# Kernel tuning notes

Hardware: AMD Instinct MI355X
Metric: run time of the kernel (lower is better)

Reference implementation:

```python
import jax, jax.numpy as jnp
import numpy as np

N_EMBD = 1024
N_HEADS = 16
B, T = 4, 2048
EPS = 1e-5


def setup_inputs() -> dict:
    key = jax.random.key(0)
    ks = jax.random.split(key, 8)
    C = N_EMBD
    s = 0.02
    return {
        "x": jax.random.normal(ks[0], (B, T, C), dtype=jnp.float32),
        "ln1_w": jnp.ones((C,), jnp.float32),
        "ln1_b": jnp.zeros((C,), jnp.float32),
        "qkv_w": jax.random.normal(ks[1], (C, 3 * C), jnp.float32) * s,
        "qkv_b": jnp.zeros((3 * C,), jnp.float32),
        "proj_w": jax.random.normal(ks[2], (C, C), jnp.float32) * s,
        "proj_b": jnp.zeros((C,), jnp.float32),
        "ln2_w": jnp.ones((C,), jnp.float32),
        "ln2_b": jnp.zeros((C,), jnp.float32),
        "ff_w1": jax.random.normal(ks[3], (C, 4 * C), jnp.float32) * s,
        "ff_b1": jnp.zeros((4 * C,), jnp.float32),
        "ff_w2": jax.random.normal(ks[4], (4 * C, C), jnp.float32) * s,
        "ff_b2": jnp.zeros((C,), jnp.float32),
    }


def _layernorm(x, w, b):
    mu = jnp.mean(x, axis=-1, keepdims=True)
    var = jnp.mean(jnp.square(x - mu), axis=-1, keepdims=True)
    return (x - mu) * jax.lax.rsqrt(var + EPS) * w + b


def _block(x, ln1_w, ln1_b, qkv_w, qkv_b, proj_w, proj_b,
           ln2_w, ln2_b, ff_w1, ff_b1, ff_w2, ff_b2):
    Bb, Tt, C = x.shape
    hd = C // N_HEADS
    h = _layernorm(x, ln1_w, ln1_b)
    qkv = h @ qkv_w + qkv_b  # [B,T,3C]
    q, k, v = jnp.split(qkv, 3, axis=-1)
    q = q.reshape(Bb, Tt, N_HEADS, hd)
    k = k.reshape(Bb, Tt, N_HEADS, hd)
    v = v.reshape(Bb, Tt, N_HEADS, hd)
    # NOTE: original scales by 1/sqrt(C) (full embed dim), not 1/sqrt(head_dim)
    att = jnp.einsum("bqhd,bkhd->bhqk", q, k) * (1.0 / C ** 0.5)
    causal = jnp.tril(jnp.ones((Tt, Tt), dtype=bool))
    att = jnp.where(causal[None, None], att, -jnp.inf)
    att = jax.nn.softmax(att, axis=-1)
    y = jnp.einsum("bhqk,bkhd->bqhd", att, v).reshape(Bb, Tt, C)
    x = x + y @ proj_w + proj_b
    h2 = _layernorm(x, ln2_w, ln2_b)
    ff = jax.nn.relu(h2 @ ff_w1 + ff_b1) @ ff_w2 + ff_b2
    return x + ff


def reference(x, ln1_w, ln1_b, qkv_w, qkv_b, proj_w, proj_b,
              ln2_w, ln2_b, ff_w1, ff_b1, ff_w2, ff_b2):
    return _block(x, ln1_w, ln1_b, qkv_w, qkv_b, proj_w, proj_b,
                  ln2_w, ln2_b, ff_w1, ff_b1, ff_w2, ff_b2)
```

## Files before the change

kernel.cpp:

```cpp
#include <hip/hip_runtime.h>


typedef __attribute__((ext_vector_type(8))) short shortx8;
typedef __attribute__((ext_vector_type(4))) float floatx4;

__device__ __forceinline__ short f2bf(float f) {
  unsigned u = __builtin_bit_cast(unsigned, f);
  u = (u + 0x7fffu + ((u >> 16) & 1u)) >> 16;
  return (short)u;
}
__device__ __forceinline__ float bf2f(short s) {
  return __builtin_bit_cast(float, (unsigned)((unsigned short)s) << 16);
}

__global__ __launch_bounds__(256)
void transpose_cast(const float* __restrict__ in, short* __restrict__ out,
                    int K, int N) {
  __shared__ float tile[32][33];
  const int n0 = blockIdx.x * 32, k0 = blockIdx.y * 32;
  const int tx = threadIdx.x & 31, ty = threadIdx.x >> 5;
  for (int i = 0; i < 32; i += 8)
    tile[ty + i][tx] = in[(size_t)(k0 + ty + i) * N + n0 + tx];
  __syncthreads();
  for (int i = 0; i < 32; i += 8)
    out[(size_t)(n0 + ty + i) * K + k0 + tx] = f2bf(tile[tx][ty + i]);
}

__global__ __launch_bounds__(256)
void layernorm_kernel(const float* __restrict__ x, const float* __restrict__ w,
                      const float* __restrict__ bta, short* __restrict__ out) {
  const int C = 1024;
  const int row = blockIdx.x;
  const float4 v = ((const float4*)(x + (size_t)row * C))[threadIdx.x];
  float s1 = v.x + v.y + v.z + v.w;
  float s2 = v.x * v.x + v.y * v.y + v.z * v.z + v.w * v.w;
  for (int m = 1; m < 64; m <<= 1) { s1 += __shfl_xor(s1, m); s2 += __shfl_xor(s2, m); }
  __shared__ float r1[4], r2[4];
  const int wid = threadIdx.x >> 6, lane = threadIdx.x & 63;
  if (lane == 0) { r1[wid] = s1; r2[wid] = s2; }
  __syncthreads();
  s1 = r1[0] + r1[1] + r1[2] + r1[3];
  s2 = r2[0] + r2[1] + r2[2] + r2[3];
  const float mean = s1 * (1.0f / C);
  const float var = s2 * (1.0f / C) - mean * mean;
  const float rs = rsqrtf(var + 1e-5f);
  const float4 wv = ((const float4*)w)[threadIdx.x];
  const float4 bv = ((const float4*)bta)[threadIdx.x];
  short4 o;
  o.x = f2bf((v.x - mean) * rs * wv.x + bv.x);
  o.y = f2bf((v.y - mean) * rs * wv.y + bv.y);
  o.z = f2bf((v.z - mean) * rs * wv.z + bv.z);
  o.w = f2bf((v.w - mean) * rs * wv.w + bv.w);
  *(short4*)(out + (size_t)row * C + threadIdx.x * 4) = o;
}

template<int FLAGS, typename OutT>
__global__ __launch_bounds__(256, 4)
void gemm_bt(const short* __restrict__ A, int lda,
             const short* __restrict__ Bt, int ldb,
             const float* __restrict__ bias, const float* __restrict__ resid,
             OutT* __restrict__ C, int M, int N, int K) {
  constexpr bool RELU = (FLAGS & 1) != 0;
  constexpr bool RESID = (FLAGS & 2) != 0;
  __shared__ short As[2][128 * 32];
  __shared__ short Bs[2][128 * 32];
  int bmi, bni;
  {
    const int nb = gridDim.x, mb = gridDim.y;
    const int g = blockIdx.x + nb * blockIdx.y;
    if ((mb & 7) == 0) {
      const int xcd = g & 7, l = g >> 3;
      bmi = xcd * (mb >> 3) + l / nb;
      bni = l % nb;
    } else { bmi = blockIdx.y; bni = blockIdx.x; }
  }
  const int bm0 = bmi * 128, bn0 = bni * 128;
  const int tid = threadIdx.x, wid = tid >> 6, lane = tid & 63;
  const int quad = lane >> 4, l15 = lane & 15;
  const int wm = wid & 1, wn = wid >> 1;
  const int srow = lane >> 2, scol = (lane & 3) * 8;
  floatx4 acc[4][4] = {};
  for (int k0 = 0; k0 < K; k0 += 64) {
    for (int i = 0; i < 2; ++i) {
      const int r0 = (wid * 2 + i) * 16;
      const short* ga = A + (size_t)(bm0 + r0 + srow) * lda + k0 + scol;
      const short* gb = Bt + (size_t)(bn0 + r0 + srow) * ldb + k0 + scol;
      __builtin_amdgcn_global_load_lds(
          (const __attribute__((address_space(1))) void*)ga,
          (__attribute__((address_space(3))) void*)&As[0][r0 * 32], 16, 0, 0);
      __builtin_amdgcn_global_load_lds(
          (const __attribute__((address_space(1))) void*)(ga + 32),
          (__attribute__((address_space(3))) void*)&As[1][r0 * 32], 16, 0, 0);
      __builtin_amdgcn_global_load_lds(
          (const __attribute__((address_space(1))) void*)gb,
          (__attribute__((address_space(3))) void*)&Bs[0][r0 * 32], 16, 0, 0);
      __builtin_amdgcn_global_load_lds(
          (const __attribute__((address_space(1))) void*)(gb + 32),
          (__attribute__((address_space(3))) void*)&Bs[1][r0 * 32], 16, 0, 0);
    }
    asm volatile("s_waitcnt vmcnt(0)" ::: "memory");
    __syncthreads();
    {
      shortx8 af[4], bfr[4];
#pragma unroll
      for (int i = 0; i < 4; ++i)
        af[i] = *(const shortx8*)&As[0][(wm * 64 + i * 16 + l15) * 32 + quad * 8];
#pragma unroll
      for (int j = 0; j < 4; ++j)
        bfr[j] = *(const shortx8*)&Bs[0][(wn * 64 + j * 16 + l15) * 32 + quad * 8];
#pragma unroll
      for (int i = 0; i < 4; ++i)
#pragma unroll
        for (int j = 0; j < 4; ++j)
          acc[i][j] = __builtin_amdgcn_mfma_f32_16x16x32_bf16(af[i], bfr[j], acc[i][j], 0, 0, 0);
    }
    {
      shortx8 af[4], bfr[4];
#pragma unroll
      for (int i = 0; i < 4; ++i)
        af[i] = *(const shortx8*)&As[1][(wm * 64 + i * 16 + l15) * 32 + quad * 8];
#pragma unroll
      for (int j = 0; j < 4; ++j)
        bfr[j] = *(const shortx8*)&Bs[1][(wn * 64 + j * 16 + l15) * 32 + quad * 8];
#pragma unroll
      for (int i = 0; i < 4; ++i)
#pragma unroll
        for (int j = 0; j < 4; ++j)
          acc[i][j] = __builtin_amdgcn_mfma_f32_16x16x32_bf16(af[i], bfr[j], acc[i][j], 0, 0, 0);
    }
    __syncthreads();
  }
#pragma unroll
  for (int i = 0; i < 4; ++i) {
    const int row = bm0 + wm * 64 + i * 16 + quad * 4;
#pragma unroll
    for (int j = 0; j < 4; ++j) {
      const int col = bn0 + wn * 64 + j * 16 + l15;
      const float bb = bias[col];
#pragma unroll
      for (int r = 0; r < 4; ++r) {
        float v = acc[i][j][r] + bb;
        if (RELU) v = fmaxf(v, 0.0f);
        if (RESID) v += resid[(size_t)(row + r) * N + col];
        if constexpr (sizeof(OutT) == 2)
          C[(size_t)(row + r) * N + col] = f2bf(v);
        else
          C[(size_t)(row + r) * N + col] = v;
      }
    }
  }
}

template<int FLAGS, typename OutT>
__global__ __launch_bounds__(256, 4)
void gemm_bt_n64(const short* __restrict__ A, int lda,
                 const short* __restrict__ Bt, int ldb,
                 const float* __restrict__ bias, const float* __restrict__ resid,
                 OutT* __restrict__ C, int M, int N, int K) {
  constexpr bool RELU = (FLAGS & 1) != 0;
  constexpr bool RESID = (FLAGS & 2) != 0;
  __shared__ short As[2][128 * 32];
  __shared__ short Bs[2][64 * 32];
  int bmi, bni;
  {
    const int nb = gridDim.x, mb = gridDim.y;
    const int g = blockIdx.x + nb * blockIdx.y;
    if ((mb & 7) == 0) {
      const int xcd = g & 7, l = g >> 3;
      bmi = xcd * (mb >> 3) + l / nb;
      bni = l % nb;
    } else { bmi = blockIdx.y; bni = blockIdx.x; }
  }
  const int bm0 = bmi * 128, bn0 = bni * 64;
  const int tid = threadIdx.x, wid = tid >> 6, lane = tid & 63;
  const int quad = lane >> 4, l15 = lane & 15;
  const int wm = wid & 1, wn = wid >> 1;
  const int srow = lane >> 2, scol = (lane & 3) * 8;
  floatx4 acc[4][2] = {};
  for (int k0 = 0; k0 < K; k0 += 64) {
    for (int i = 0; i < 2; ++i) {
      const int r0 = (wid * 2 + i) * 16;
      const short* ga = A + (size_t)(bm0 + r0 + srow) * lda + k0 + scol;
      __builtin_amdgcn_global_load_lds(
          (const __attribute__((address_space(1))) void*)ga,
          (__attribute__((address_space(3))) void*)&As[0][r0 * 32], 16, 0, 0);
      __builtin_amdgcn_global_load_lds(
          (const __attribute__((address_space(1))) void*)(ga + 32),
          (__attribute__((address_space(3))) void*)&As[1][r0 * 32], 16, 0, 0);
    }
    {
      const int r0b = wid * 16;
      const short* gb = Bt + (size_t)(bn0 + r0b + srow) * ldb + k0 + scol;
      __builtin_amdgcn_global_load_lds(
          (const __attribute__((address_space(1))) void*)gb,
          (__attribute__((address_space(3))) void*)&Bs[0][r0b * 32], 16, 0, 0);
      __builtin_amdgcn_global_load_lds(
          (const __attribute__((address_space(1))) void*)(gb + 32),
          (__attribute__((address_space(3))) void*)&Bs[1][r0b * 32], 16, 0, 0);
    }
    asm volatile("s_waitcnt vmcnt(0)" ::: "memory");
    __syncthreads();
    {
      shortx8 af[4], bfr[2];
#pragma unroll
      for (int i = 0; i < 4; ++i)
        af[i] = *(const shortx8*)&As[0][(wm * 64 + i * 16 + l15) * 32 + quad * 8];
#pragma unroll
      for (int j = 0; j < 2; ++j)
        bfr[j] = *(const shortx8*)&Bs[0][(wn * 32 + j * 16 + l15) * 32 + quad * 8];
#pragma unroll
      for (int i = 0; i < 4; ++i)
#pragma unroll
        for (int j = 0; j < 2; ++j)
          acc[i][j] = __builtin_amdgcn_mfma_f32_16x16x32_bf16(af[i], bfr[j], acc[i][j], 0, 0, 0);
    }
    {
      shortx8 af[4], bfr[2];
#pragma unroll
      for (int i = 0; i < 4; ++i)
        af[i] = *(const shortx8*)&As[1][(wm * 64 + i * 16 + l15) * 32 + quad * 8];
#pragma unroll
      for (int j = 0; j < 2; ++j)
        bfr[j] = *(const shortx8*)&Bs[1][(wn * 32 + j * 16 + l15) * 32 + quad * 8];
#pragma unroll
      for (int i = 0; i < 4; ++i)
#pragma unroll
        for (int j = 0; j < 2; ++j)
          acc[i][j] = __builtin_amdgcn_mfma_f32_16x16x32_bf16(af[i], bfr[j], acc[i][j], 0, 0, 0);
    }
    __syncthreads();
  }
#pragma unroll
  for (int i = 0; i < 4; ++i) {
    const int row = bm0 + wm * 64 + i * 16 + quad * 4;
#pragma unroll
    for (int j = 0; j < 2; ++j) {
      const int col = bn0 + wn * 32 + j * 16 + l15;
      const float bb = bias[col];
#pragma unroll
      for (int r = 0; r < 4; ++r) {
        float v = acc[i][j][r] + bb;
        if (RELU) v = fmaxf(v, 0.0f);
        if (RESID) v += resid[(size_t)(row + r) * N + col];
        if constexpr (sizeof(OutT) == 2)
          C[(size_t)(row + r) * N + col] = f2bf(v);
        else
          C[(size_t)(row + r) * N + col] = v;
      }
    }
  }
}

#define ATTN_SLOTS 80
#define ATTN_SLOT_SH 4224

__global__ __launch_bounds__(256)
void attention_chunk(const short* __restrict__ qkv, short* __restrict__ y,
                     float* __restrict__ part) {
  constexpr int T = 2048, C = 1024, HD = 64, S3 = 3072;
  __shared__ short Ks[64 * 72];
  __shared__ short Vt[64 * 72];
  __shared__ short Ps[4][16 * 72];
  const int x = blockIdx.x, h = blockIdx.y, b = blockIdx.z;
  int qb, ch;
  if (x < 8)       { qb = x;                 ch = 0; }
  else if (x < 24) { qb = 8 + ((x - 8) >> 1);  ch = (x - 8) & 1; }
  else if (x < 48) { qb = 16 + (x - 24) / 3;   ch = (x - 24) % 3; }
  else             { qb = 24 + ((x - 48) >> 2); ch = (x - 48) & 3; }
  const int kt0 = ch * 8;
  const int kt1 = min(kt0 + 8, qb + 1);
  const int tid = threadIdx.x, wid = tid >> 6, lane = tid & 63;
  const int quad = lane >> 4, l15 = lane & 15;
  const size_t base = (size_t)b * T * S3;
  const int q0 = qb * 64 + wid * 16;
  const short* Qp = qkv + base + (size_t)(q0 + l15) * S3 + h * HD;
  const shortx8 qf0 = *(const shortx8*)(Qp + quad * 8);
  const shortx8 qf1 = *(const shortx8*)(Qp + 32 + quad * 8);
  floatx4 o[4] = {};
  float lsum[4] = {0.f, 0.f, 0.f, 0.f};
  const float scale2 = 0.03125f * 1.44269504088896f;
  const int skey = tid >> 2, sd = (tid & 3) * 16;
  const int vkp = tid & 31, vdb = tid >> 5;
  const int vkE = (vkp >> 4) * 32 + (vkp & 15);
  const short* Kbase = qkv + base + C + h * HD;
  const short* Vbase = qkv + base + 2 * C + h * HD;
  shortx8 pk0, pk1, pv0, pv1;
  {
    const short* Kp = Kbase + (size_t)(kt0 * 64 + skey) * S3 + sd;
    pk0 = *(const shortx8*)Kp;
    pk1 = *(const shortx8*)(Kp + 8);
    const short* Vp = Vbase + (size_t)(kt0 * 64 + vkE) * S3 + vdb * 8;
    pv0 = *(const shortx8*)Vp;
    pv1 = *(const shortx8*)(Vp + 16 * S3);
  }
  for (int kt = kt0; kt < kt1; ++kt) {
    const int key0 = kt * 64;
    __syncthreads();
    *(shortx8*)&Ks[skey * 72 + sd] = pk0;
    *(shortx8*)&Ks[skey * 72 + sd + 8] = pk1;
#pragma unroll
    for (int j = 0; j < 8; ++j) {
      short2 pr = make_short2(pv0[j], pv1[j]);
      *(short2*)&Vt[(vdb * 8 + j) * 72 + 2 * vkp] = pr;
    }
    __syncthreads();
    if (kt + 1 < kt1) {
      const int kn = key0 + 64;
      const short* Kp = Kbase + (size_t)(kn + skey) * S3 + sd;
      pk0 = *(const shortx8*)Kp;
      pk1 = *(const shortx8*)(Kp + 8);
      const short* Vp = Vbase + (size_t)(kn + vkE) * S3 + vdb * 8;
      pv0 = *(const shortx8*)Vp;
      pv1 = *(const shortx8*)(Vp + 16 * S3);
    }
    floatx4 s[4];
#pragma unroll
    for (int nt = 0; nt < 4; ++nt) {
      const short* kb = &Ks[(nt * 16 + l15) * 72 + quad * 8];
      floatx4 a = {};
      a = __builtin_amdgcn_mfma_f32_16x16x32_bf16(qf0, *(const shortx8*)kb, a, 0, 0, 0);
      a = __builtin_amdgcn_mfma_f32_16x16x32_bf16(qf1, *(const shortx8*)(kb + 32), a, 0, 0, 0);
      s[nt] = a;
    }
    short* pw = &Ps[wid][0];
    if (kt != qb) {
#pragma unroll
      for (int r = 0; r < 4; ++r) {
        const float p0 = __builtin_amdgcn_exp2f(s[0][r] * scale2);
        const float p1 = __builtin_amdgcn_exp2f(s[1][r] * scale2);
        const float p2 = __builtin_amdgcn_exp2f(s[2][r] * scale2);
        const float p3 = __builtin_amdgcn_exp2f(s[3][r] * scale2);
        lsum[r] += (p0 + p1) + (p2 + p3);
        unsigned w0, w1;
        asm("v_cvt_pk_bf16_f32 %0, %1, %2" : "=v"(w0) : "v"(p0), "v"(p1));
        asm("v_cvt_pk_bf16_f32 %0, %1, %2" : "=v"(w1) : "v"(p2), "v"(p3));
        unsigned* prow = (unsigned*)&pw[(quad * 4 + r) * 72];
        prow[l15] = w0;
        prow[16 + l15] = w1;
      }
    } else {
#pragma unroll
      for (int r = 0; r < 4; ++r) {
        const int q = q0 + quad * 4 + r;
        float pr[4];
#pragma unroll
        for (int nt = 0; nt < 4; ++nt) {
          float sv = s[nt][r] * scale2;
          if (key0 + nt * 16 + l15 > q) sv = -INFINITY;
          pr[nt] = __builtin_amdgcn_exp2f(sv);
        }
        lsum[r] += (pr[0] + pr[1]) + (pr[2] + pr[3]);
        unsigned w0, w1;
        asm("v_cvt_pk_bf16_f32 %0, %1, %2" : "=v"(w0) : "v"(pr[0]), "v"(pr[1]));
        asm("v_cvt_pk_bf16_f32 %0, %1, %2" : "=v"(w1) : "v"(pr[2]), "v"(pr[3]));
        unsigned* prow = (unsigned*)&pw[(quad * 4 + r) * 72];
        prow[l15] = w0;
        prow[16 + l15] = w1;
      }
    }
    asm volatile("s_waitcnt lgkmcnt(0)" ::: "memory");
#pragma unroll
    for (int kf = 0; kf < 2; ++kf) {
      const shortx8 pa = *(const shortx8*)&Ps[wid][l15 * 72 + kf * 32 + quad * 8];
#pragma unroll
      for (int dt = 0; dt < 4; ++dt) {
        const shortx8 vb = *(const shortx8*)&Vt[(dt * 16 + l15) * 72 + kf * 32 + quad * 8];
        o[dt] = __builtin_amdgcn_mfma_f32_16x16x32_bf16(pa, vb, o[dt], 0, 0, 0);
      }
    }
  }
  float ls[4];
#pragma unroll
  for (int r = 0; r < 4; ++r) {
    float s = lsum[r];
    for (int off = 1; off < 16; off <<= 1) s += __shfl_xor(s, off);
    ls[r] = s;
  }
  if (x < 8) {
    float inv[4];
#pragma unroll
    for (int r = 0; r < 4; ++r) inv[r] = __builtin_amdgcn_rcpf(ls[r]);
#pragma unroll
    for (int dt = 0; dt < 4; ++dt)
#pragma unroll
      for (int r = 0; r < 4; ++r) {
        const int q = q0 + quad * 4 + r;
        y[((size_t)b * T + q) * C + h * HD + dt * 16 + l15] =
            f2bf(o[dt][r] * inv[r]);
      }
  } else {
    short* pp = (short*)part +
                ((size_t)(b * 16 + h) * ATTN_SLOTS + x) * ATTN_SLOT_SH;
    float* pl = (float*)(pp + 4096);
    const int qw = wid * 16;
#pragma unroll
    for (int dt = 0; dt < 4; ++dt)
#pragma unroll
      for (int r = 0; r < 4; ++r)
        pp[(qw + quad * 4 + r) * 64 + dt * 16 + l15] = f2bf(o[dt][r]);
    if (l15 == 0)
#pragma unroll
      for (int r = 0; r < 4; ++r)
        pl[qw + quad * 4 + r] = ls[r];
  }
}

__global__ __launch_bounds__(256)
void attn_reduce(const float* __restrict__ part, short* __restrict__ y) {
  constexpr int T = 2048, C = 1024;
  const int qb = 8 + blockIdx.x, h = blockIdx.y, b = blockIdx.z;
  const int c = qb / 8 + 1;
  int slot0;
  if (qb < 16)      slot0 = 8 + 2 * (qb - 8);
  else if (qb < 24) slot0 = 24 + 3 * (qb - 16);
  else              slot0 = 48 + 4 * (qb - 24);
  const short* rb = (const short*)part +
                    ((size_t)(b * 16 + h) * ATTN_SLOTS + slot0) * ATTN_SLOT_SH;
  const int t = threadIdx.x;
  const int q = t >> 2, dg = (t & 3) * 16;
  float acc[16] = {};
  float ls = 0.f;
  for (int ci = 0; ci < c; ++ci) {
    const short* pp = rb + (size_t)ci * ATTN_SLOT_SH;
    const shortx8 v0 = *(const shortx8*)(pp + q * 64 + dg);
    const shortx8 v1 = *(const shortx8*)(pp + q * 64 + dg + 8);
#pragma unroll
    for (int i = 0; i < 8; ++i) {
      acc[i] += bf2f(v0[i]);
      acc[8 + i] += bf2f(v1[i]);
    }
    ls += *(const float*)(pp + 4096 + 2 * q);
  }
  const float inv = __builtin_amdgcn_rcpf(ls);
  short o16[16];
#pragma unroll
  for (int i = 0; i < 16; ++i) o16[i] = f2bf(acc[i] * inv);
  short* yp = y + ((size_t)b * T + qb * 64 + q) * C + h * 64 + dg;
  *(shortx8*)yp = *(shortx8*)&o16[0];
  *(shortx8*)(yp + 8) = *(shortx8*)&o16[8];
}

__global__ __launch_bounds__(256)
void attention_kernel(const short* __restrict__ qkv, short* __restrict__ y) {
  constexpr int T = 2048, C = 1024, HD = 64, S3 = 3072;
  __shared__ short Ks[64 * 72];
  __shared__ short Vt[64 * 72];
  __shared__ short Ps[4][16 * 72];
  const int qb = blockIdx.x, h = blockIdx.y, b = blockIdx.z;
  const int tid = threadIdx.x, wid = tid >> 6, lane = tid & 63;
  const int quad = lane >> 4, l15 = lane & 15;
  const size_t base = (size_t)b * T * S3;
  const int q0 = qb * 64 + wid * 16;
  const short* Qp = qkv + base + (size_t)(q0 + l15) * S3 + h * HD;
  const shortx8 qf0 = *(const shortx8*)(Qp + quad * 8);
  const shortx8 qf1 = *(const shortx8*)(Qp + 32 + quad * 8);
  floatx4 o[4] = {};
  float lsum[4] = {0.f, 0.f, 0.f, 0.f};
  const float scale2 = 0.03125f * 1.44269504088896f;
  const int skey = tid >> 2, sd = (tid & 3) * 16;
  const int vkp = tid & 31, vdb = tid >> 5;
  for (int kt = 0; kt <= qb; ++kt) {
    const int key0 = kt * 64;
    __syncthreads();
    {
      const short* Kp = qkv + base + (size_t)(key0 + skey) * S3 + C + h * HD + sd;
      shortx8 ka = *(const shortx8*)Kp;
      shortx8 kb = *(const shortx8*)(Kp + 8);
      *(shortx8*)&Ks[skey * 72 + sd] = ka;
      *(shortx8*)&Ks[skey * 72 + sd + 8] = kb;
      const short* Vp = qkv + base + (size_t)(key0 + 2 * vkp) * S3 + 2 * C + h * HD + vdb * 8;
      shortx8 va = *(const shortx8*)Vp;
      shortx8 vb = *(const shortx8*)(Vp + S3);
#pragma unroll
      for (int j = 0; j < 8; ++j) {
        short2 pr = make_short2(va[j], vb[j]);
        *(short2*)&Vt[(vdb * 8 + j) * 72 + 2 * vkp] = pr;
      }
    }
    __syncthreads();
    floatx4 s[4];
#pragma unroll
    for (int nt = 0; nt < 4; ++nt) {
      const short* kb = &Ks[(nt * 16 + l15) * 72 + quad * 8];
      floatx4 a = {};
      a = __builtin_amdgcn_mfma_f32_16x16x32_bf16(qf0, *(const shortx8*)kb, a, 0, 0, 0);
      a = __builtin_amdgcn_mfma_f32_16x16x32_bf16(qf1, *(const shortx8*)(kb + 32), a, 0, 0, 0);
      s[nt] = a;
    }
    short* pw = &Ps[wid][0];
    const bool diag = (kt == qb);
#pragma unroll
    for (int nt = 0; nt < 4; ++nt)
#pragma unroll
      for (int r = 0; r < 4; ++r) {
        float sv = s[nt][r] * scale2;
        if (diag) {
          const int key = key0 + nt * 16 + l15;
          const int q = q0 + quad * 4 + r;
          if (key > q) sv = -INFINITY;
        }
        const float p = __builtin_amdgcn_exp2f(sv);
        lsum[r] += p;
        pw[(quad * 4 + r) * 72 + nt * 16 + l15] = f2bf(p);
      }
    asm volatile("s_waitcnt lgkmcnt(0)" ::: "memory");
#pragma unroll
    for (int kf = 0; kf < 2; ++kf) {
      const shortx8 pa = *(const shortx8*)&Ps[wid][l15 * 72 + kf * 32 + quad * 8];
#pragma unroll
      for (int dt = 0; dt < 4; ++dt) {
        const shortx8 vb = *(const shortx8*)&Vt[(dt * 16 + l15) * 72 + kf * 32 + quad * 8];
        o[dt] = __builtin_amdgcn_mfma_f32_16x16x32_bf16(pa, vb, o[dt], 0, 0, 0);
      }
    }
  }
  float inv[4];
#pragma unroll
  for (int r = 0; r < 4; ++r) {
    float s = lsum[r];
    for (int off = 1; off < 16; off <<= 1) s += __shfl_xor(s, off);
    inv[r] = __builtin_amdgcn_rcpf(s);
  }
#pragma unroll
  for (int dt = 0; dt < 4; ++dt)
#pragma unroll
    for (int r = 0; r < 4; ++r) {
      const int q = q0 + quad * 4 + r;
      y[((size_t)b * T + q) * C + h * HD + dt * 16 + l15] = f2bf(o[dt][r] * inv[r]);
    }
}

extern "C" void kernel_launch(void* const* d_in, const int* in_sizes, int n_in,
                              void* d_out, int out_size, void* d_ws, size_t ws_size,
                              hipStream_t stream) {
  const float* x      = (const float*)d_in[0];
  const float* ln1_w  = (const float*)d_in[1];
  const float* ln1_b  = (const float*)d_in[2];
  const float* qkv_w  = (const float*)d_in[3];
  const float* qkv_b  = (const float*)d_in[4];
  const float* proj_w = (const float*)d_in[5];
  const float* proj_b = (const float*)d_in[6];
  const float* ln2_w  = (const float*)d_in[7];
  const float* ln2_b  = (const float*)d_in[8];
  const float* ff_w1  = (const float*)d_in[9];
  const float* ff_b1  = (const float*)d_in[10];
  const float* ff_w2  = (const float*)d_in[11];
  const float* ff_b2  = (const float*)d_in[12];
  float* out = (float*)d_out;

  char* p = (char*)d_ws;
  short* wT_qkv  = (short*)p; p += (size_t)3072 * 1024 * 2;
  short* wT_proj = (short*)p; p += (size_t)1024 * 1024 * 2;
  short* wT_ff1  = (short*)p; p += (size_t)4096 * 1024 * 2;
  short* wT_ff2  = (short*)p; p += (size_t)1024 * 4096 * 2;
  short* act16   = (short*)p; p += (size_t)8192 * 1024 * 2;
  short* big     = (short*)p; p += (size_t)8192 * 4096 * 2;
  float* part    = (float*)p;
  const size_t need = (size_t)(p - (char*)d_ws) +
                      (size_t)64 * ATTN_SLOTS * ATTN_SLOT_SH * 2;
  const bool split = (ws_size >= need);

  transpose_cast<<<dim3(96, 32), 256, 0, stream>>>(qkv_w, wT_qkv, 1024, 3072);
  transpose_cast<<<dim3(32, 32), 256, 0, stream>>>(proj_w, wT_proj, 1024, 1024);
  transpose_cast<<<dim3(128, 32), 256, 0, stream>>>(ff_w1, wT_ff1, 1024, 4096);
  transpose_cast<<<dim3(32, 128), 256, 0, stream>>>(ff_w2, wT_ff2, 4096, 1024);

  layernorm_kernel<<<8192, 256, 0, stream>>>(x, ln1_w, ln1_b, act16);
  gemm_bt<0, short><<<dim3(24, 64), 256, 0, stream>>>(
      act16, 1024, wT_qkv, 1024, qkv_b, nullptr, big, 8192, 3072, 1024);
  if (split) {
    attention_chunk<<<dim3(ATTN_SLOTS, 16, 4), 256, 0, stream>>>(big, act16, part);
    attn_reduce<<<dim3(24, 16, 4), 256, 0, stream>>>(part, act16);
  } else {
    attention_kernel<<<dim3(32, 16, 4), 256, 0, stream>>>(big, act16);
  }
  gemm_bt_n64<2, float><<<dim3(16, 64), 256, 0, stream>>>(
      act16, 1024, wT_proj, 1024, proj_b, x, out, 8192, 1024, 1024);
  layernorm_kernel<<<8192, 256, 0, stream>>>(out, ln2_w, ln2_b, act16);
  gemm_bt<1, short><<<dim3(32, 64), 256, 0, stream>>>(
      act16, 1024, wT_ff1, 1024, ff_b1, nullptr, big, 8192, 4096, 1024);
  gemm_bt_n64<2, float><<<dim3(16, 64), 256, 0, stream>>>(
      big, 4096, wT_ff2, 4096, ff_b2, out, out, 8192, 1024, 4096);
}
```

Measured before the change: 522.8 us.

## Use 128x128 tiles with K=128 steps for ff2 and generic gemm for proj

Replaces the 128x64-tile GEMM used for the output projection and second FFN matmul. The projection now uses the existing 128x128 gemm_bt kernel, and FFN2 uses a new kernel with 128x128 tiles that stages 128 K-elements per iteration, halving barrier and wait rounds per K step. Larger tiles raise arithmetic intensity and cut redundant global loads, but the grid drops to 512 blocks, 64 KB of LDS per block may limit occupancy, and 16 accumulators per wave add register pressure.

```diff
diff --git a/kernel.cpp b/kernel.cpp
--- a/kernel.cpp
+++ b/kernel.cpp
@@ -153,14 +153,14 @@
 
 template<int FLAGS, typename OutT>
 __global__ __launch_bounds__(256, 4)
-void gemm_bt_n64(const short* __restrict__ A, int lda,
-                 const short* __restrict__ Bt, int ldb,
-                 const float* __restrict__ bias, const float* __restrict__ resid,
-                 OutT* __restrict__ C, int M, int N, int K) {
+void gemm_bt_k128(const short* __restrict__ A, int lda,
+                  const short* __restrict__ Bt, int ldb,
+                  const float* __restrict__ bias, const float* __restrict__ resid,
+                  OutT* __restrict__ C, int M, int N, int K) {
   constexpr bool RELU = (FLAGS & 1) != 0;
   constexpr bool RESID = (FLAGS & 2) != 0;
-  __shared__ short As[2][128 * 32];
-  __shared__ short Bs[2][64 * 32];
+  __shared__ short As[4][128 * 32];
+  __shared__ short Bs[4][128 * 32];
   int bmi, bni;
   {
     const int nb = gridDim.x, mb = gridDim.y;
@@ -171,61 +171,98 @@
       bni = l % nb;
     } else { bmi = blockIdx.y; bni = blockIdx.x; }
   }
-  const int bm0 = bmi * 128, bn0 = bni * 64;
+  const int bm0 = bmi * 128, bn0 = bni * 128;
   const int tid = threadIdx.x, wid = tid >> 6, lane = tid & 63;
   const int quad = lane >> 4, l15 = lane & 15;
   const int wm = wid & 1, wn = wid >> 1;
   const int srow = lane >> 2, scol = (lane & 3) * 8;
-  floatx4 acc[4][2] = {};
-  for (int k0 = 0; k0 < K; k0 += 64) {
+  floatx4 acc[4][4] = {};
+  for (int k0 = 0; k0 < K; k0 += 128) {
     for (int i = 0; i < 2; ++i) {
       const int r0 = (wid * 2 + i) * 16;
       const short* ga = A + (size_t)(bm0 + r0 + srow) * lda + k0 + scol;
+      const short* gb = Bt + (size_t)(bn0 + r0 + srow) * ldb + k0 + scol;
       __builtin_amdgcn_global_load_lds(
           (const __attribute__((address_space(1))) void*)ga,
           (__attribute__((address_space(3))) void*)&As[0][r0 * 32], 16, 0, 0);
       __builtin_amdgcn_global_load_lds(
           (const __attribute__((address_space(1))) void*)(ga + 32),
           (__attribute__((address_space(3))) void*)&As[1][r0 * 32], 16, 0, 0);
-    }
+      __builtin_amdgcn_global_load_lds(
+          (const __attribute__((address_space(1))) void*)(ga + 64),
+          (__attribute__((address_space(3))) void*)&As[2][r0 * 32], 16, 0, 0);
+      __builtin_amdgcn_global_load_lds(
+          (const __attribute__((address_space(1))) void*)(ga + 96),
+          (__attribute__((address_space(3))) void*)&As[3][r0 * 32], 16, 0, 0);
+      __builtin_amdgcn_global_load_lds(
+          (const __attribute__((address_space(1))) void*)gb,
+          (__attribute__((address_space(3))) void*)&Bs[0][r0 * 32], 16, 0, 0);
+      __builtin_amdgcn_global_load_lds(
+          (const __attribute__((address_space(1))) void*)(gb + 32),
+          (__attribute__((address_space(3))) void*)&Bs[1][r0 * 32], 16, 0, 0);
+      __builtin_amdgcn_global_load_lds(
+          (const __attribute__((address_space(1))) void*)(gb + 64),
+          (__attribute__((address_space(3))) void*)&Bs[2][r0 * 32], 16, 0, 0);
+      __builtin_amdgcn_global_load_lds(
+          (const __attribute__((address_space(1))) void*)(gb + 96),
+          (__attribute__((address_space(3))) void*)&Bs[3][r0 * 32], 16, 0, 0);
+    }
+    asm volatile("s_waitcnt vmcnt(0)" ::: "memory");
+    __syncthreads();
     {
-      const int r0b = wid * 16;
-      const short* gb = Bt + (size_t)(bn0 + r0b + srow) * ldb + k0 + scol;
-      __builtin_amdgcn_global_load_lds(
-          (const __attribute__((address_space(1))) void*)gb,
-          (__attribute__((address_space(3))) void*)&Bs[0][r0b * 32], 16, 0, 0);
-      __builtin_amdgcn_global_load_lds(
-          (const __attribute__((address_space(1))) void*)(gb + 32),
-          (__attribute__((address_space(3))) void*)&Bs[1][r0b * 32], 16, 0, 0);
-    }
-    asm volatile("s_waitcnt vmcnt(0)" ::: "memory");
-    __syncthreads();
+      shortx8 af[4], bfr[4];
+#pragma unroll
+      for (int i = 0; i < 4; ++i)
+        af[i] = *(const shortx8*)&As[0][(wm * 64 + i * 16 + l15) * 32 + quad * 8];
+#pragma unroll
+      for (int j = 0; j < 4; ++j)
+        bfr[j] = *(const shortx8*)&Bs[0][(wn * 64 + j * 16 + l15) * 32 + quad * 8];
+#pragma unroll
+      for (int i = 0; i < 4; ++i)
+#pragma unroll
+        for (int j = 0; j < 4; ++j)
+          acc[i][j] = __builtin_amdgcn_mfma_f32_16x16x32_bf16(af[i], bfr[j], acc[i][j], 0, 0, 0);
+    }
     {
-      shortx8 af[4], bfr[2];
-#pragma unroll
-      for (int i = 0; i < 4; ++i)
-        af[i] = *(const shortx8*)&As[0][(wm * 64 + i * 16 + l15) * 32 + quad * 8];
-#pragma unroll
-      for (int j = 0; j < 2; ++j)
-        bfr[j] = *(const shortx8*)&Bs[0][(wn * 32 + j * 16 + l15) * 32 + quad * 8];
-#pragma unroll
-      for (int i = 0; i < 4; ++i)
-#pragma unroll
-        for (int j = 0; j < 2; ++j)
+      shortx8 af[4], bfr[4];
+#pragma unroll
+      for (int i = 0; i < 4; ++i)
+        af[i] = *(const shortx8*)&As[1][(wm * 64 + i * 16 + l15) * 32 + quad * 8];
+#pragma unroll
+      for (int j = 0; j < 4; ++j)
+        bfr[j] = *(const shortx8*)&Bs[1][(wn * 64 + j * 16 + l15) * 32 + quad * 8];
+#pragma unroll
+      for (int i = 0; i < 4; ++i)
+#pragma unroll
+        for (int j = 0; j < 4; ++j)
           acc[i][j] = __builtin_amdgcn_mfma_f32_16x16x32_bf16(af[i], bfr[j], acc[i][j], 0, 0, 0);
     }
     {
-      shortx8 af[4], bfr[2];
-#pragma unroll
-      for (int i = 0; i < 4; ++i)
-        af[i] = *(const shortx8*)&As[1][(wm * 64 + i * 16 + l15) * 32 + quad * 8];
-#pragma unroll
-      for (int j = 0; j < 2; ++j)
-        bfr[j] = *(const shortx8*)&Bs[1][(wn * 32 + j * 16 + l15) * 32 + quad * 8];
-#pragma unroll
-      for (int i = 0; i < 4; ++i)
-#pragma unroll
-        for (int j = 0; j < 2; ++j)
+      shortx8 af[4], bfr[4];
+#pragma unroll
+      for (int i = 0; i < 4; ++i)
+        af[i] = *(const shortx8*)&As[2][(wm * 64 + i * 16 + l15) * 32 + quad * 8];
+#pragma unroll
+      for (int j = 0; j < 4; ++j)
+        bfr[j] = *(const shortx8*)&Bs[2][(wn * 64 + j * 16 + l15) * 32 + quad * 8];
+#pragma unroll
+      for (int i = 0; i < 4; ++i)
+#pragma unroll
+        for (int j = 0; j < 4; ++j)
+          acc[i][j] = __builtin_amdgcn_mfma_f32_16x16x32_bf16(af[i], bfr[j], acc[i][j], 0, 0, 0);
+    }
+    {
+      shortx8 af[4], bfr[4];
+#pragma unroll
+      for (int i = 0; i < 4; ++i)
+        af[i] = *(const shortx8*)&As[3][(wm * 64 + i * 16 + l15) * 32 + quad * 8];
+#pragma unroll
+      for (int j = 0; j < 4; ++j)
+        bfr[j] = *(const shortx8*)&Bs[3][(wn * 64 + j * 16 + l15) * 32 + quad * 8];
+#pragma unroll
+      for (int i = 0; i < 4; ++i)
+#pragma unroll
+        for (int j = 0; j < 4; ++j)
           acc[i][j] = __builtin_amdgcn_mfma_f32_16x16x32_bf16(af[i], bfr[j], acc[i][j], 0, 0, 0);
     }
     __syncthreads();
@@ -234,8 +271,8 @@
   for (int i = 0; i < 4; ++i) {
     const int row = bm0 + wm * 64 + i * 16 + quad * 4;
 #pragma unroll
-    for (int j = 0; j < 2; ++j) {
-      const int col = bn0 + wn * 32 + j * 16 + l15;
+    for (int j = 0; j < 4; ++j) {
+      const int col = bn0 + wn * 64 + j * 16 + l15;
       const float bb = bias[col];
 #pragma unroll
       for (int r = 0; r < 4; ++r) {
@@ -574,11 +611,11 @@
   } else {
     attention_kernel<<<dim3(32, 16, 4), 256, 0, stream>>>(big, act16);
   }
-  gemm_bt_n64<2, float><<<dim3(16, 64), 256, 0, stream>>>(
+  gemm_bt<2, float><<<dim3(8, 64), 256, 0, stream>>>(
       act16, 1024, wT_proj, 1024, proj_b, x, out, 8192, 1024, 1024);
   layernorm_kernel<<<8192, 256, 0, stream>>>(out, ln2_w, ln2_b, act16);
   gemm_bt<1, short><<<dim3(32, 64), 256, 0, stream>>>(
       act16, 1024, wT_ff1, 1024, ff_b1, nullptr, big, 8192, 4096, 1024);
-  gemm_bt_n64<2, float><<<dim3(16, 64), 256, 0, stream>>>(
+  gemm_bt_k128<2, float><<<dim3(8, 64), 256, 0, stream>>>(
       big, 4096, wT_ff2, 4096, ff_b2, out, out, 8192, 1024, 4096);
 }
```

After: 482.0 us, median of 2. 7.8% less time.
